# Optimization experiments

Measured on AMD Instinct MI355X. Metric: run time of the kernel, lower is better.

The kernel has to match this reference:

```python
import jax, jax.numpy as jnp
import numpy as np
jax.config.update("jax_enable_x64", True)

# BLS12-377 Fr modulus (scalar field of G1)
P_INT = 0x12ab655e9a2ca55660b44d1e5c37b00159aa76fed00000010a11800000000001
NL = 8  # number of 32-bit limbs used internally
MASK = np.uint64(0xffffffff)

def _limbs32(x):
    return [np.uint64((x >> (32 * i)) & 0xffffffff) for i in range(NL)]

P_L = _limbs32(P_INT)                       # modulus limbs
R2_L = _limbs32((1 << 512) % P_INT)         # R^2 mod p, R = 2^256 (to_mont multiplier)
INV32 = np.uint64((-pow(P_INT, -1, 1 << 32)) % (1 << 32))  # -p^{-1} mod 2^32

def _split(x):
    # [..., 4] int64 (little-endian 64-bit limbs) -> list of 8 uint64 arrays holding 32-bit limbs, LSB first
    x = x.astype(jnp.uint64)
    out = []
    for k in range(4):
        out.append(x[..., k] & MASK)
        out.append(x[..., k] >> 32)
    return out

def _join(limbs):
    # list of 8 32-bit limbs -> [..., 4] uint64 64-bit limbs
    words = [limbs[2 * k] | (limbs[2 * k + 1] << 32) for k in range(4)]
    return jnp.stack(words, axis=-1)

def _cond_sub(t, extra):
    # branchless: r = t - p; select r when (extra != 0) or t >= p (no final borrow)
    borrow = jnp.zeros_like(t[0])
    r = []
    for j in range(NL):
        d = t[j] - P_L[j] - borrow            # uint64 wraparound encodes borrow in high bits
        r.append(d & MASK)
        borrow = (d >> 32) & jnp.uint64(1)
    use = (extra != 0) | (borrow == 0)
    return [jnp.where(use, r[j], t[j]) for j in range(NL)]

def _montmul(a, b):
    # CIOS Montgomery multiplication with 32-bit limbs in uint64 accumulators.
    # a: list of 8 uint64 arrays (<2^32); b: list of 8 uint64 scalars/arrays (<2^32)
    z = jnp.zeros_like(a[0])
    t = [z] * (NL + 2)
    for i in range(NL):
        c = z
        for j in range(NL):
            s = t[j] + a[i] * b[j] + c        # < 2^64, no overflow
            t[j] = s & MASK
            c = s >> 32
        s = t[NL] + c
        t[NL] = s & MASK
        t[NL + 1] = s >> 32
        m = (t[0] * INV32) & MASK
        s = t[0] + m * P_L[0]
        c = s >> 32
        for j in range(1, NL):
            s = t[j] + m * P_L[j] + c
            t[j - 1] = s & MASK
            c = s >> 32
        s = t[NL] + c
        t[NL - 1] = s & MASK
        t[NL] = t[NL + 1] + (s >> 32)
        t[NL + 1] = z
    return _cond_sub(t[:NL], t[NL])

def _modadd(a, b):
    # limbwise add with carry, then conditional subtract of p (Montgomery add == modular add)
    c = jnp.zeros_like(a[0])
    s_l = []
    for j in range(NL):
        s = a[j] + b[j] + c
        s_l.append(s & MASK)
        c = s >> 32
    return _cond_sub(s_l, c)

def setup_inputs() -> dict:
    key = jax.random.key(0)
    k1, k2 = jax.random.split(key)
    N = 4194304
    # each limb < 2^31 guarantees the 256-bit value < 2^223 < p
    input1 = jax.random.randint(k1, (N, 4), 0, 2147483648, dtype=jnp.int64)
    input2 = jax.random.randint(k2, (N, 4), 0, 2147483648, dtype=jnp.int64)
    return {"input1": input1, "input2": input2}

def reference(input1, input2):
    a = _split(input1)
    b = _split(input2)
    am = _montmul(a, R2_L)   # F.to_mont(input1): x * R mod p via MontMul(x, R^2)
    bm = _montmul(b, R2_L)   # F.to_mont(input2)
    return _join(_modadd(am, bm))  # F.add_mont
```

## Files before the change

### kernel.cpp

```cpp
#include <hip/hip_runtime.h>
#include <stdint.h>


#define MASK32 0xffffffffull

namespace {

constexpr uint32_t PL[8] = {
  0x00000001u, 0x0a118000u, 0xd0000001u, 0x59aa76feu,
  0x5c37b001u, 0x60b44d1eu, 0x9a2ca556u, 0x12ab655eu
};

struct U256 { uint32_t l[8]; };

constexpr bool geq_p(const U256& x) {
  for (int i = 7; i >= 0; --i) {
    if (x.l[i] != PL[i]) return x.l[i] > PL[i];
  }
  return true;
}

constexpr U256 pow2_mod(int e) {
  U256 x{};
  for (int i = 0; i < 8; ++i) x.l[i] = 0;
  x.l[7] = 0x10000000u;
  for (int it = 0; it < e - 252; ++it) {
    uint32_t carry = 0;
    for (int j = 0; j < 8; ++j) {
      uint32_t nc = x.l[j] >> 31;
      x.l[j] = (x.l[j] << 1) | carry;
      carry = nc;
    }
    if (geq_p(x)) {
      uint64_t borrow = 0;
      for (int j = 0; j < 8; ++j) {
        uint64_t d = (uint64_t)x.l[j] - (uint64_t)PL[j] - borrow;
        x.l[j] = (uint32_t)d;
        borrow = (d >> 32) & 1ull;
      }
    }
  }
  return x;
}

constexpr U256 D0 = pow2_mod(320);
constexpr U256 D1 = pow2_mod(384);
constexpr U256 D2 = pow2_mod(448);
constexpr U256 D3 = pow2_mod(512);

}

__global__ __launch_bounds__(256) void fr_tomont_add_kernel(
    const int4* __restrict__ in1,
    const int4* __restrict__ in2,
    int4* __restrict__ out,
    int n) {
  int idx = blockIdx.x * blockDim.x + threadIdx.x;
  if (idx >= n) return;

  int4 av = in1[idx];
  int4 bv = in2[idx];

  uint32_t s0 = (uint32_t)av.x + (uint32_t)bv.x;
  uint32_t s1 = (uint32_t)av.y + (uint32_t)bv.y;
  uint32_t s2 = (uint32_t)av.z + (uint32_t)bv.z;
  uint32_t s3 = (uint32_t)av.w + (uint32_t)bv.w;

  uint64_t t[9];

  {
    uint64_t c = 0;
#pragma unroll
    for (int j = 0; j < 8; ++j) {
      uint64_t x = (uint64_t)s0 * (uint64_t)D0.l[j] + c;
      t[j] = x & MASK32;
      c = x >> 32;
    }
    t[8] = c;
  }

  {
    const uint32_t* Dk[3] = {D1.l, D2.l, D3.l};
    const uint32_t sk[3] = {s1, s2, s3};
#pragma unroll
    for (int k = 0; k < 3; ++k) {
      uint64_t c = 0;
#pragma unroll
      for (int j = 0; j < 8; ++j) {
        uint64_t x = t[j] + (uint64_t)sk[k] * (uint64_t)Dk[k][j] + c;
        t[j] = x & MASK32;
        c = x >> 32;
      }
      t[8] += c;
    }
  }

  {
    uint32_t m = (uint32_t)0u - (uint32_t)t[0];
    uint64_t c = ((uint32_t)t[0] != 0u) ? 1ull : 0ull;
#pragma unroll
    for (int j = 1; j < 8; ++j) {
      uint64_t x = t[j] + (uint64_t)m * (uint64_t)PL[j] + c;
      t[j - 1] = x & MASK32;
      c = x >> 32;
    }
    t[7] = t[8] + c;
  }

  {
    uint32_t m = (uint32_t)0u - (uint32_t)t[0];
    uint64_t c = ((uint32_t)t[0] != 0u) ? 1ull : 0ull;
#pragma unroll
    for (int j = 1; j < 8; ++j) {
      uint64_t x = t[j] + (uint64_t)m * (uint64_t)PL[j] + c;
      t[j - 1] = x & MASK32;
      c = x >> 32;
    }
    t[7] = c;
  }

  uint32_t d[8];
  uint64_t borrow = 0;
#pragma unroll
  for (int j = 0; j < 8; ++j) {
    uint64_t x = t[j] - (uint64_t)PL[j] - borrow;
    d[j] = (uint32_t)x;
    borrow = (x >> 32) & 1ull;
  }
  bool use = (borrow == 0);
  uint32_t r0 = use ? d[0] : (uint32_t)t[0];
  uint32_t r2 = use ? d[2] : (uint32_t)t[2];
  uint32_t r4 = use ? d[4] : (uint32_t)t[4];
  uint32_t r6 = use ? d[6] : (uint32_t)t[6];

  out[idx] = make_int4((int)r0, (int)r2, (int)r4, (int)r6);
}

extern "C" void kernel_launch(void* const* d_in, const int* in_sizes, int n_in,
                              void* d_out, int out_size, void* d_ws, size_t ws_size,
                              hipStream_t stream) {
  const int4* in1 = (const int4*)d_in[0];
  const int4* in2 = (const int4*)d_in[1];
  int4* out = (int4*)d_out;
  int n = in_sizes[0] / 4;

  const int block = 256;
  const int grid = (n + block - 1) / block;
  fr_tomont_add_kernel<<<grid, block, 0, stream>>>(in1, in2, out, n);
}
```

Before: 35.43 us.

## Use grid-stride loop with software-prefetched loads and nontemporal stores

Turns the one-element-per-thread kernel into a grid-stride loop in which each thread handles about eight elements and loads the next element's inputs before computing the current one, to overlap memory latency with the Montgomery arithmetic. Output is written with nontemporal stores. The 9th accumulator limb is narrowed to 32 bits and the first reduction carry is computed arithmetically instead of with a compare. The kernel also gets an occupancy hint in launch_bounds. The smaller grid lowers parallelism and the prefetch raises register pressure.

```diff
diff --git a/kernel.cpp b/kernel.cpp
--- a/kernel.cpp
+++ b/kernel.cpp
@@ -3,6 +3,8 @@
 
 
 #define MASK32 0xffffffffull
+
+typedef int v4i __attribute__((ext_vector_type(4)));
 
 namespace {
 
@@ -50,23 +52,14 @@
 
 }
 
-__global__ __launch_bounds__(256) void fr_tomont_add_kernel(
-    const int4* __restrict__ in1,
-    const int4* __restrict__ in2,
-    int4* __restrict__ out,
-    int n) {
-  int idx = blockIdx.x * blockDim.x + threadIdx.x;
-  if (idx >= n) return;
-
-  int4 av = in1[idx];
-  int4 bv = in2[idx];
-
+__device__ __forceinline__ v4i fr_tomont_add_one(const v4i av, const v4i bv) {
   uint32_t s0 = (uint32_t)av.x + (uint32_t)bv.x;
   uint32_t s1 = (uint32_t)av.y + (uint32_t)bv.y;
   uint32_t s2 = (uint32_t)av.z + (uint32_t)bv.z;
   uint32_t s3 = (uint32_t)av.w + (uint32_t)bv.w;
 
-  uint64_t t[9];
+  uint64_t t[8];
+  uint32_t t8;
 
   {
     uint64_t c = 0;
@@ -76,7 +69,7 @@
       t[j] = x & MASK32;
       c = x >> 32;
     }
-    t[8] = c;
+    t8 = (uint32_t)c;
   }
 
   {
@@ -91,25 +84,27 @@
         t[j] = x & MASK32;
         c = x >> 32;
       }
-      t[8] += c;
+      t8 += (uint32_t)c;
     }
   }
 
   {
     uint32_t m = (uint32_t)0u - (uint32_t)t[0];
-    uint64_t c = ((uint32_t)t[0] != 0u) ? 1ull : 0ull;
+    uint64_t x0 = t[0] + (uint64_t)m;
+    uint64_t c = x0 >> 32;
 #pragma unroll
     for (int j = 1; j < 8; ++j) {
       uint64_t x = t[j] + (uint64_t)m * (uint64_t)PL[j] + c;
       t[j - 1] = x & MASK32;
       c = x >> 32;
     }
-    t[7] = t[8] + c;
+    t[7] = (uint64_t)(t8 + (uint32_t)c);
   }
 
   {
     uint32_t m = (uint32_t)0u - (uint32_t)t[0];
-    uint64_t c = ((uint32_t)t[0] != 0u) ? 1ull : 0ull;
+    uint64_t x0 = t[0] + (uint64_t)m;
+    uint64_t c = x0 >> 32;
 #pragma unroll
     for (int j = 1; j < 8; ++j) {
       uint64_t x = t[j] + (uint64_t)m * (uint64_t)PL[j] + c;
@@ -128,23 +123,55 @@
     borrow = (x >> 32) & 1ull;
   }
   bool use = (borrow == 0);
-  uint32_t r0 = use ? d[0] : (uint32_t)t[0];
-  uint32_t r2 = use ? d[2] : (uint32_t)t[2];
-  uint32_t r4 = use ? d[4] : (uint32_t)t[4];
-  uint32_t r6 = use ? d[6] : (uint32_t)t[6];
+  v4i o;
+  o.x = (int)(use ? d[0] : (uint32_t)t[0]);
+  o.y = (int)(use ? d[2] : (uint32_t)t[2]);
+  o.z = (int)(use ? d[4] : (uint32_t)t[4]);
+  o.w = (int)(use ? d[6] : (uint32_t)t[6]);
+  return o;
+}
 
-  out[idx] = make_int4((int)r0, (int)r2, (int)r4, (int)r6);
+__global__ __launch_bounds__(256, 8) void fr_tomont_add_kernel(
+    const v4i* __restrict__ in1,
+    const v4i* __restrict__ in2,
+    v4i* __restrict__ out,
+    int n) {
+  int i = blockIdx.x * blockDim.x + threadIdx.x;
+  int stride = gridDim.x * blockDim.x;
+  if (i >= n) return;
+
+  v4i a = in1[i];
+  v4i b = in2[i];
+
+  for (;;) {
+    int next = i + stride;
+    bool more = next < n;
+    v4i an, bn;
+    if (more) {
+      an = in1[next];
+      bn = in2[next];
+    }
+
+    v4i o = fr_tomont_add_one(a, b);
+    __builtin_nontemporal_store(o, out + i);
+
+    if (!more) break;
+    i = next;
+    a = an;
+    b = bn;
+  }
 }
 
 extern "C" void kernel_launch(void* const* d_in, const int* in_sizes, int n_in,
                               void* d_out, int out_size, void* d_ws, size_t ws_size,
                               hipStream_t stream) {
-  const int4* in1 = (const int4*)d_in[0];
-  const int4* in2 = (const int4*)d_in[1];
-  int4* out = (int4*)d_out;
+  const v4i* in1 = (const v4i*)d_in[0];
+  const v4i* in2 = (const v4i*)d_in[1];
+  v4i* out = (v4i*)d_out;
   int n = in_sizes[0] / 4;
 
   const int block = 256;
-  const int grid = (n + block - 1) / block;
+  const int elems_per_thread = 8;
+  int grid = (n + block * elems_per_thread - 1) / (block * elems_per_thread);
   fr_tomont_add_kernel<<<grid, block, 0, stream>>>(in1, in2, out, n);
 }
```

After: 39.31 us. 10.9% more time.
